# Kernel tuning notes

Measured on AMD Instinct MI355X. Metric: run time of the kernel, lower is better.

The kernel has to match this reference:

```python
import jax, jax.numpy as jnp
import numpy as np

B, T = 1, 1024
V, E, H, HKV, DH = 32000, 1024, 16, 4, 64
L, R = 2, 2            # n_layer, n_recurrent
ROPE = 32              # head_dim * rotary_pct (0.5)
EPS = 1e-5


def _layer_norm(x, g, b):
    mu = jnp.mean(x, axis=-1, keepdims=True)
    var = jnp.mean((x - mu) ** 2, axis=-1, keepdims=True)
    return (x - mu) * jax.lax.rsqrt(var + EPS) * g + b


def _rotate_half(x):
    x1, x2 = jnp.split(x, 2, axis=-1)
    return jnp.concatenate([-x2, x1], axis=-1)


def _rope_cache(t):
    theta = 1.0 / (10000.0 ** (jnp.arange(0, ROPE, 2, dtype=jnp.float32) / ROPE))
    freqs = jnp.arange(t, dtype=jnp.float32)[:, None] * theta[None, :]  # [t, ROPE/2]
    cos = jnp.concatenate([jnp.cos(freqs), jnp.cos(freqs)], axis=-1)    # [t, ROPE]
    sin = jnp.concatenate([jnp.sin(freqs), jnp.sin(freqs)], axis=-1)
    return cos, sin


def _attn(x, Wq, Wk, Wv, Wo, gate, cos, sin):
    b, t, c = x.shape
    q = (x @ Wq).reshape(b, t, H, DH).transpose(0, 2, 1, 3)     # [b,H,t,D]
    k = (x @ Wk).reshape(b, t, HKV, DH).transpose(0, 2, 1, 3)   # [b,Hkv,t,D]
    v = (x @ Wv).reshape(b, t, HKV, DH).transpose(0, 2, 1, 3)
    c4, s4 = cos[None, None, :t, :], sin[None, None, :t, :]
    q_r, q_p = q[..., :ROPE], q[..., ROPE:]
    k_r, k_p = k[..., :ROPE], k[..., ROPE:]
    q = jnp.concatenate([q_r * c4 + _rotate_half(q_r) * s4, q_p], axis=-1)
    k = jnp.concatenate([k_r * c4 + _rotate_half(k_r) * s4, k_p], axis=-1)
    # GQA: repeat kv heads
    k = jnp.repeat(k, H // HKV, axis=1)
    v = jnp.repeat(v, H // HKV, axis=1)
    att = jnp.einsum('bhtd,bhsd->bhts', q, k) * (DH ** -0.5)
    causal = jnp.tril(jnp.ones((t, t), dtype=bool))
    att = jnp.where(causal[None, None], att, -jnp.inf)
    att = jax.nn.softmax(att, axis=-1)
    # learned per-head sigmoid-threshold sparsifying gate
    thr = jax.nn.sigmoid(gate)[None, :, None, None]
    att = att * (att >= thr).astype(att.dtype)
    y = jnp.einsum('bhts,bhsd->bhtd', att, v).transpose(0, 2, 1, 3).reshape(b, t, c)
    return y @ Wo


def reference(embed, ln1_g, ln1_b, Wq, Wk, Wv, Wo, gate, ln2_g, ln2_b, W1, W2, lnf_g, lnf_b, idx, targets):
    x = embed[idx]                      # [B,T,E]
    cos, sin = _rope_cache(T)
    for _ in range(R):
        for l in range(L):
            x = x + _attn(_layer_norm(x, ln1_g[l], ln1_b[l]), Wq[l], Wk[l], Wv[l], Wo[l], gate[l], cos, sin)
            h = _layer_norm(x, ln2_g[l], ln2_b[l])
            x = x + jax.nn.gelu(h @ W1[l], approximate=False) @ W2[l]
    x = _layer_norm(x, lnf_g, lnf_b)
    logits = x @ embed.T                # tied lm_head
    logp = jax.nn.log_softmax(logits, axis=-1)
    loss = -jnp.mean(jnp.take_along_axis(logp, targets[..., None], axis=-1))
    return logits, loss


def setup_inputs():
    key = jax.random.key(0)
    ks = jax.random.split(key, 9)
    s = 0.02
    return {
        'embed': jax.random.normal(ks[0], (V, E), jnp.float32) * s,
        'ln1_g': jnp.ones((L, E), jnp.float32), 'ln1_b': jnp.zeros((L, E), jnp.float32),
        'Wq': jax.random.normal(ks[1], (L, E, E), jnp.float32) * s,
        'Wk': jax.random.normal(ks[2], (L, E, HKV * DH), jnp.float32) * s,
        'Wv': jax.random.normal(ks[3], (L, E, HKV * DH), jnp.float32) * s,
        'Wo': jax.random.normal(ks[4], (L, E, E), jnp.float32) * s,
        'gate': jnp.zeros((L, H), jnp.float32),
        'ln2_g': jnp.ones((L, E), jnp.float32), 'ln2_b': jnp.zeros((L, E), jnp.float32),
        'W1': jax.random.normal(ks[5], (L, E, 4 * E), jnp.float32) * s,
        'W2': jax.random.normal(ks[6], (L, 4 * E, E), jnp.float32) * s,
        'lnf_g': jnp.ones((E,), jnp.float32), 'lnf_b': jnp.zeros((E,), jnp.float32),
        'idx': jax.random.randint(ks[7], (B, T), 0, V, dtype=jnp.int32),
        'targets': jax.random.randint(ks[8], (B, T), 0, V, dtype=jnp.int32),
    }
```

## Files before the change

kernel.cpp:

```cpp
#include <hip/hip_runtime.h>
#include <math.h>

#define TT 1024
#define VV 32000
#define EE 1024
#define NH 16
#define NKVH 4
#define DHEAD 64
#define QKVN 1536
#define FF 4096
#define LEPS 1e-5f

typedef __attribute__((ext_vector_type(8))) short short8;
typedef __attribute__((ext_vector_type(4))) float floatx4;

__device__ __forceinline__ ushort f2bf(float f) {
    unsigned x = __float_as_uint(f);
    unsigned r = (x + 0x7fffu + ((x >> 16) & 1u)) >> 16;
    return (ushort)r;
}
__device__ __forceinline__ float bf2f(ushort u) {
    return __uint_as_float(((unsigned)u) << 16);
}

__device__ __forceinline__ float block_reduce_sum(float v, float* red) {
    int tid = threadIdx.x;
    red[tid] = v; __syncthreads();
    for (int off = 128; off > 0; off >>= 1) {
        if (tid < off) red[tid] += red[tid + off];
        __syncthreads();
    }
    float r = red[0];
    __syncthreads();
    return r;
}
__device__ __forceinline__ float block_reduce_max(float v, float* red) {
    int tid = threadIdx.x;
    red[tid] = v; __syncthreads();
    for (int off = 128; off > 0; off >>= 1) {
        if (tid < off) red[tid] = fmaxf(red[tid], red[tid + off]);
        __syncthreads();
    }
    float r = red[0];
    __syncthreads();
    return r;
}

__global__ __launch_bounds__(256) void convert_bf16_kernel(const float* __restrict__ src,
                                                           ushort* __restrict__ dst, long n4) {
    long i = (long)blockIdx.x * 256 + threadIdx.x;
    if (i >= n4) return;
    float4 f = ((const float4*)src)[i];
    ushort u[4] = { f2bf(f.x), f2bf(f.y), f2bf(f.z), f2bf(f.w) };
    ((uint2*)dst)[i] = *(uint2*)u;
}

__global__ __launch_bounds__(256) void transpose_bf16_kernel(const float* __restrict__ W,
                                                             ushort* __restrict__ dst,
                                                             int N, int K) {
    __shared__ float tile[32][33];
    int n0 = blockIdx.x * 32, k0 = blockIdx.y * 32;
    int tx = threadIdx.x & 31, ty = threadIdx.x >> 5;
    for (int i = ty; i < 32; i += 8) tile[i][tx] = W[(long)(k0 + i) * N + n0 + tx];
    __syncthreads();
    for (int i = ty; i < 32; i += 8)
        dst[(long)(n0 + i) * K + k0 + tx] = f2bf(tile[tx][i]);
}

__global__ __launch_bounds__(256) void gather_kernel(const float* __restrict__ embed,
                                                     const int* __restrict__ idx,
                                                     float* __restrict__ x) {
    int t = blockIdx.x;
    long r = idx[t];
    const float4* src = (const float4*)(embed + r * EE);
    float4* dst = (float4*)(x + (long)t * EE);
    for (int i = threadIdx.x; i < EE / 4; i += 256) dst[i] = src[i];
}

__global__ __launch_bounds__(256) void ln_kernel(const float* __restrict__ x,
                                                 const float* __restrict__ g,
                                                 const float* __restrict__ b,
                                                 ushort* __restrict__ out) {
    __shared__ float red[256];
    int t = blockIdx.x;
    const float* xr = x + (long)t * EE;
    float s = 0.f;
    for (int i = threadIdx.x; i < EE; i += 256) s += xr[i];
    float mu = block_reduce_sum(s, red) * (1.f / EE);
    float vs = 0.f;
    for (int i = threadIdx.x; i < EE; i += 256) { float d = xr[i] - mu; vs += d * d; }
    float var = block_reduce_sum(vs, red) * (1.f / EE);
    float rstd = rsqrtf(var + LEPS);
    ushort* orow = out + (long)t * EE;
    for (int i = threadIdx.x; i < EE; i += 256)
        orow[i] = f2bf((xr[i] - mu) * rstd * g[i] + b[i]);
}

__global__ __launch_bounds__(256) void rope_kernel(ushort* __restrict__ q, int nheads, int rowstride) {
    int idx = blockIdx.x * 256 + threadIdx.x;
    int total = TT * nheads * 16;
    if (idx >= total) return;
    int i = idx & 15;
    int h = (idx >> 4) % nheads;
    int t = idx / (16 * nheads);
    float theta = expf(-(float)i * (9.210340371976184f / 16.f));
    float ang = (float)t * theta;
    float c = cosf(ang), s = sinf(ang);
    ushort* p = q + (long)t * rowstride + h * DHEAD;
    float a = bf2f(p[i]), bb = bf2f(p[i + 16]);
    p[i]      = f2bf(a * c - bb * s);
    p[i + 16] = f2bf(bb * c + a * s);
}

template<bool GELU_ACT, bool ADD, bool OUTBF>
__global__ __launch_bounds__(256) void gemm_bf16(const ushort* __restrict__ A,
                                                 const ushort* __restrict__ B,
                                                 void* __restrict__ Cv,
                                                 int M, int N, int K) {
    __shared__ char lds[16384];
    const int tid = threadIdx.x;
    const int lane = tid & 63;
    const int w = tid >> 6;

    const int nwg = gridDim.x;
    const int lin = blockIdx.x;
    const int q8 = nwg >> 3, r8 = nwg & 7;
    const int xcd = lin & 7, loc = lin >> 3;
    const int wg = (xcd < r8 ? xcd * (q8 + 1) : r8 * (q8 + 1) + (xcd - r8) * q8) + loc;
    const int MB = M >> 7;
    const int row0 = (wg % MB) * 128;
    const int col0 = (wg / MB) * 128;

    const int nsl = gridDim.y;
    const int kslice = K / nsl;
    const long koff = (long)blockIdx.y * kslice;

    const char* ga[2]; const char* gb[2];
    char* la[2]; char* lb[2];
    #pragma unroll
    for (int r = 0; r < 2; ++r) {
        int c = r * 256 + tid;
        ga[r] = (const char*)A + ((long)(row0 + (c >> 2)) * K + koff) * 2 + (c & 3) * 16;
        gb[r] = (const char*)B + ((long)(col0 + (c >> 2)) * K + koff) * 2 + (c & 3) * 16;
        int wc = r * 256 + w * 64;
        la[r] = lds + wc * 16;
        lb[r] = lds + 8192 + wc * 16;
    }

    floatx4 acc[4][4];
    #pragma unroll
    for (int i = 0; i < 4; ++i)
        #pragma unroll
        for (int j = 0; j < 4; ++j) acc[i][j] = {0.f, 0.f, 0.f, 0.f};

    const int mbase = (w >> 1) * 64;
    const int nbase = (w & 1) * 64;
    const int lr = lane & 15;
    const int ko = (lane >> 4) * 16;

    for (int k0 = 0; k0 < kslice; k0 += 32) {
        #pragma unroll
        for (int r = 0; r < 2; ++r) {
            __builtin_amdgcn_global_load_lds(
                (const __attribute__((address_space(1))) void*)ga[r],
                (__attribute__((address_space(3))) void*)la[r], 16, 0, 0);
            __builtin_amdgcn_global_load_lds(
                (const __attribute__((address_space(1))) void*)gb[r],
                (__attribute__((address_space(3))) void*)lb[r], 16, 0, 0);
            ga[r] += 64; gb[r] += 64;
        }
        __syncthreads();
        short8 af[4], bfr[4];
        #pragma unroll
        for (int i = 0; i < 4; ++i)
            af[i] = *(const short8*)(lds + (mbase + i * 16 + lr) * 64 + ko);
        #pragma unroll
        for (int j = 0; j < 4; ++j)
            bfr[j] = *(const short8*)(lds + 8192 + (nbase + j * 16 + lr) * 64 + ko);
        #pragma unroll
        for (int i = 0; i < 4; ++i)
            #pragma unroll
            for (int j = 0; j < 4; ++j)
                acc[i][j] = __builtin_amdgcn_mfma_f32_16x16x32_bf16(af[i], bfr[j], acc[i][j], 0, 0, 0);
        __syncthreads();
    }

    const int orow = (lane >> 4) * 4;
    const int ocol = lane & 15;
    #pragma unroll
    for (int i = 0; i < 4; ++i) {
        #pragma unroll
        for (int j = 0; j < 4; ++j) {
            #pragma unroll
            for (int r = 0; r < 4; ++r) {
                long off = (long)(row0 + mbase + i * 16 + orow + r) * N
                         + (col0 + nbase + j * 16 + ocol);
                float v = acc[i][j][r];
                if (GELU_ACT) v = 0.5f * v * (1.f + erff(v * 0.70710678118654752f));
                if (OUTBF) {
                    ((ushort*)Cv)[off] = f2bf(v);
                } else {
                    float* C = (float*)Cv + (long)blockIdx.y * (long)M * N;
                    if (ADD) C[off] += v; else C[off] = v;
                }
            }
        }
    }
}

__global__ __launch_bounds__(256) void reduce_add_kernel(const float* __restrict__ part,
                                                         float* __restrict__ x,
                                                         long n4, int SK) {
    long i = (long)blockIdx.x * 256 + threadIdx.x;
    if (i >= n4) return;
    float4 s = ((const float4*)part)[i];
    for (int k = 1; k < SK; ++k) {
        float4 t = ((const float4*)part)[i + (long)k * n4];
        s.x += t.x; s.y += t.y; s.z += t.z; s.w += t.w;
    }
    float4 d = ((float4*)x)[i];
    d.x += s.x; d.y += s.y; d.z += s.z; d.w += s.w;
    ((float4*)x)[i] = d;
}

__global__ __launch_bounds__(256) void scores_gemm(const ushort* __restrict__ qkv,
                                                   float* __restrict__ scores) {
    __shared__ char lds[16384];
    const int tid = threadIdx.x;
    const int lane = tid & 63;
    const int w = tid >> 6;
    const int col0 = blockIdx.x * 128, row0 = blockIdx.y * 128, h = blockIdx.z;
    if (col0 > row0) return;

    const ushort* A = qkv + h * DHEAD;
    const ushort* B = qkv + EE + (h >> 2) * DHEAD;

    const char* ga[2]; const char* gb[2];
    char* la[2]; char* lb[2];
    #pragma unroll
    for (int r = 0; r < 2; ++r) {
        int c = r * 256 + tid;
        ga[r] = (const char*)A + (long)(row0 + (c >> 2)) * QKVN * 2 + (c & 3) * 16;
        gb[r] = (const char*)B + (long)(col0 + (c >> 2)) * QKVN * 2 + (c & 3) * 16;
        int wc = r * 256 + w * 64;
        la[r] = lds + wc * 16;
        lb[r] = lds + 8192 + wc * 16;
    }

    floatx4 acc[4][4];
    #pragma unroll
    for (int i = 0; i < 4; ++i)
        #pragma unroll
        for (int j = 0; j < 4; ++j) acc[i][j] = {0.f, 0.f, 0.f, 0.f};

    const int mbase = (w >> 1) * 64;
    const int nbase = (w & 1) * 64;
    const int lr = lane & 15;
    const int ko = (lane >> 4) * 16;

    for (int k0 = 0; k0 < DHEAD; k0 += 32) {
        #pragma unroll
        for (int r = 0; r < 2; ++r) {
            __builtin_amdgcn_global_load_lds(
                (const __attribute__((address_space(1))) void*)ga[r],
                (__attribute__((address_space(3))) void*)la[r], 16, 0, 0);
            __builtin_amdgcn_global_load_lds(
                (const __attribute__((address_space(1))) void*)gb[r],
                (__attribute__((address_space(3))) void*)lb[r], 16, 0, 0);
            ga[r] += 64; gb[r] += 64;
        }
        __syncthreads();
        short8 af[4], bfr[4];
        #pragma unroll
        for (int i = 0; i < 4; ++i)
            af[i] = *(const short8*)(lds + (mbase + i * 16 + lr) * 64 + ko);
        #pragma unroll
        for (int j = 0; j < 4; ++j)
            bfr[j] = *(const short8*)(lds + 8192 + (nbase + j * 16 + lr) * 64 + ko);
        #pragma unroll
        for (int i = 0; i < 4; ++i)
            #pragma unroll
            for (int j = 0; j < 4; ++j)
                acc[i][j] = __builtin_amdgcn_mfma_f32_16x16x32_bf16(af[i], bfr[j], acc[i][j], 0, 0, 0);
        __syncthreads();
    }

    float* C = scores + (long)h * TT * TT;
    const int orow = (lane >> 4) * 4;
    const int ocol = lane & 15;
    #pragma unroll
    for (int i = 0; i < 4; ++i)
        #pragma unroll
        for (int j = 0; j < 4; ++j)
            #pragma unroll
            for (int r = 0; r < 4; ++r)
                C[(long)(row0 + mbase + i * 16 + orow + r) * TT
                  + (col0 + nbase + j * 16 + ocol)] = acc[i][j][r];
}

__global__ __launch_bounds__(256) void softmax_gate_kernel(float* __restrict__ scores,
                                                           const float* __restrict__ gate) {
    __shared__ float sc[TT];
    __shared__ float red[256];
    int h = blockIdx.x;
    int t = blockIdx.y;
    int tid = threadIdx.x;
    float* row = scores + (long)h * TT * TT + (long)t * TT;

    float lmax = -INFINITY;
    for (int s = tid; s <= t; s += 256) {
        float v = row[s] * 0.125f;
        sc[s] = v;
        lmax = fmaxf(lmax, v);
    }
    float mx = block_reduce_max(lmax, red);
    float lsum = 0.f;
    for (int s = tid; s <= t; s += 256) {
        float e = expf(sc[s] - mx);
        sc[s] = e;
        lsum += e;
    }
    float sum = block_reduce_sum(lsum, red);
    float inv = 1.f / sum;
    float thr = 1.f / (1.f + expf(-gate[h]));

    ushort* prow = (ushort*)row;
    for (int s = tid; s < TT; s += 256) {
        float p = (s <= t) ? sc[s] * inv : 0.f;
        p = (p >= thr) ? p : 0.f;
        prow[s] = f2bf(p);
    }
}

__global__ __launch_bounds__(256) void vtrans_kernel(const ushort* __restrict__ qkv,
                                                     ushort* __restrict__ VT) {
    __shared__ ushort tile[32][33];
    int s0 = blockIdx.x * 32, d0 = blockIdx.y * 32;
    int tx = threadIdx.x & 31, ty = threadIdx.x >> 5;
    for (int i = ty; i < 32; i += 8)
        tile[i][tx] = qkv[(long)(s0 + i) * QKVN + (EE + NKVH * DHEAD) + d0 + tx];
    __syncthreads();
    for (int i = ty; i < 32; i += 8)
        VT[(long)(d0 + i) * TT + s0 + tx] = tile[tx][i];
}

__global__ __launch_bounds__(256) void pv_gemm(const float* __restrict__ scores,
                                               const ushort* __restrict__ VT,
                                               ushort* __restrict__ y) {
    __shared__ char lds[12288];
    const int tid = threadIdx.x;
    const int lane = tid & 63;
    const int w = tid >> 6;
    const int row0 = blockIdx.x * 128, h = blockIdx.y;

    const char* Pb = (const char*)(scores + (long)h * TT * TT);
    const char* Bv = (const char*)(VT + (long)(h >> 2) * DHEAD * TT);

    const char* ga[2]; char* la[2];
    #pragma unroll
    for (int r = 0; r < 2; ++r) {
        int c = r * 256 + tid;
        ga[r] = Pb + (long)(row0 + (c >> 2)) * 4096 + (c & 3) * 16;
        la[r] = lds + (r * 256 + w * 64) * 16;
    }
    const char* gb = Bv + (long)(tid >> 2) * 2048 + (tid & 3) * 16;
    char* lb = lds + 8192 + (w * 64) * 16;

    floatx4 acc[2][4];
    #pragma unroll
    for (int i = 0; i < 2; ++i)
        #pragma unroll
        for (int j = 0; j < 4; ++j) acc[i][j] = {0.f, 0.f, 0.f, 0.f};

    const int mbase = w * 32;
    const int lr = lane & 15;
    const int ko = (lane >> 4) * 16;

    for (int k0 = 0; k0 < TT; k0 += 32) {
        #pragma unroll
        for (int r = 0; r < 2; ++r) {
            __builtin_amdgcn_global_load_lds(
                (const __attribute__((address_space(1))) void*)ga[r],
                (__attribute__((address_space(3))) void*)la[r], 16, 0, 0);
            ga[r] += 64;
        }
        __builtin_amdgcn_global_load_lds(
            (const __attribute__((address_space(1))) void*)gb,
            (__attribute__((address_space(3))) void*)lb, 16, 0, 0);
        gb += 64;
        __syncthreads();
        short8 af[2], bfr[4];
        #pragma unroll
        for (int i = 0; i < 2; ++i)
            af[i] = *(const short8*)(lds + (mbase + i * 16 + lr) * 64 + ko);
        #pragma unroll
        for (int j = 0; j < 4; ++j)
            bfr[j] = *(const short8*)(lds + 8192 + (j * 16 + lr) * 64 + ko);
        #pragma unroll
        for (int i = 0; i < 2; ++i)
            #pragma unroll
            for (int j = 0; j < 4; ++j)
                acc[i][j] = __builtin_amdgcn_mfma_f32_16x16x32_bf16(af[i], bfr[j], acc[i][j], 0, 0, 0);
        __syncthreads();
    }

    const int orow = (lane >> 4) * 4;
    const int ocol = lane & 15;
    #pragma unroll
    for (int i = 0; i < 2; ++i)
        #pragma unroll
        for (int j = 0; j < 4; ++j)
            #pragma unroll
            for (int r = 0; r < 4; ++r)
                y[(long)(row0 + mbase + i * 16 + orow + r) * EE
                  + h * DHEAD + j * 16 + ocol] = f2bf(acc[i][j][r]);
}

__global__ __launch_bounds__(256) void row_loss_kernel(const float* __restrict__ logits,
                                                       const int* __restrict__ targets,
                                                       float* __restrict__ row_loss) {
    __shared__ float red[256];
    int t = blockIdx.x;
    const float* lr = logits + (long)t * VV;
    float lmax = -INFINITY;
    for (int i = threadIdx.x; i < VV; i += 256) lmax = fmaxf(lmax, lr[i]);
    float mx = block_reduce_max(lmax, red);
    float ls = 0.f;
    for (int i = threadIdx.x; i < VV; i += 256) ls += expf(lr[i] - mx);
    float sum = block_reduce_sum(ls, red);
    if (threadIdx.x == 0)
        row_loss[t] = logf(sum) + mx - lr[targets[t]];
}

__global__ __launch_bounds__(256) void final_loss_kernel(const float* __restrict__ row_loss,
                                                         float* __restrict__ out) {
    __shared__ float red[256];
    float s = 0.f;
    for (int i = threadIdx.x; i < TT; i += 256) s += row_loss[i];
    float tot = block_reduce_sum(s, red);
    if (threadIdx.x == 0) out[0] = tot * (1.f / TT);
}

extern "C" void kernel_launch(void* const* d_in, const int* in_sizes, int n_in,
                              void* d_out, int out_size, void* d_ws, size_t ws_size,
                              hipStream_t stream) {
    const float* embed = (const float*)d_in[0];
    const float* ln1_g = (const float*)d_in[1];
    const float* ln1_b = (const float*)d_in[2];
    const float* Wq    = (const float*)d_in[3];
    const float* Wk    = (const float*)d_in[4];
    const float* Wv    = (const float*)d_in[5];
    const float* Wo    = (const float*)d_in[6];
    const float* gate  = (const float*)d_in[7];
    const float* ln2_g = (const float*)d_in[8];
    const float* ln2_b = (const float*)d_in[9];
    const float* W1    = (const float*)d_in[10];
    const float* W2    = (const float*)d_in[11];
    const float* lnf_g = (const float*)d_in[12];
    const float* lnf_b = (const float*)d_in[13];
    const int*   idx   = (const int*)d_in[14];
    const int*   tgt   = (const int*)d_in[15];
    float* out = (float*)d_out;

    char* p = (char*)d_ws;
    float*  x      = (float*)p;  p += (long)TT * EE * 4;
    ushort* xn     = (ushort*)p; p += (long)TT * EE * 2;
    ushort* qkvb   = (ushort*)p; p += (long)TT * QKVN * 2;
    ushort* y      = (ushort*)p; p += (long)TT * EE * 2;
    ushort* h1     = (ushort*)p; p += (long)TT * FF * 2;
    float*  rls    = (float*)p;  p += (long)TT * 4;
    ushort* VT     = (ushort*)p; p += (long)NKVH * DHEAD * TT * 2;
    float*  scores = (float*)p;  p += (long)NH * TT * TT * 4;
    ushort* wqkvT  = (ushort*)p; p += (long)2 * QKVN * EE * 2;
    ushort* woT    = (ushort*)p; p += (long)2 * EE * EE * 2;
    ushort* w1T    = (ushort*)p; p += (long)2 * FF * EE * 2;
    ushort* w2T    = (ushort*)p; p += (long)2 * EE * FF * 2;
    ushort* embB   = (ushort*)p; p += (long)VV * EE * 2;

    float* gpart = scores;

    convert_bf16_kernel<<<((long)VV * EE / 4 + 255) / 256, 256, 0, stream>>>(embed, embB, (long)VV * EE / 4);
    for (int l = 0; l < 2; ++l) {
        transpose_bf16_kernel<<<dim3(EE / 32, EE / 32), 256, 0, stream>>>(
            Wq + (long)l * EE * EE, wqkvT + (long)l * QKVN * EE, EE, EE);
        transpose_bf16_kernel<<<dim3(NKVH * DHEAD / 32, EE / 32), 256, 0, stream>>>(
            Wk + (long)l * EE * NKVH * DHEAD, wqkvT + (long)l * QKVN * EE + (long)EE * EE, NKVH * DHEAD, EE);
        transpose_bf16_kernel<<<dim3(NKVH * DHEAD / 32, EE / 32), 256, 0, stream>>>(
            Wv + (long)l * EE * NKVH * DHEAD, wqkvT + (long)l * QKVN * EE + (long)(EE + NKVH * DHEAD) * EE, NKVH * DHEAD, EE);
        transpose_bf16_kernel<<<dim3(EE / 32, EE / 32), 256, 0, stream>>>(
            Wo + (long)l * EE * EE, woT + (long)l * EE * EE, EE, EE);
        transpose_bf16_kernel<<<dim3(FF / 32, EE / 32), 256, 0, stream>>>(
            W1 + (long)l * EE * FF, w1T + (long)l * FF * EE, FF, EE);
        transpose_bf16_kernel<<<dim3(EE / 32, FF / 32), 256, 0, stream>>>(
            W2 + (long)l * FF * EE, w2T + (long)l * EE * FF, EE, FF);
    }

    gather_kernel<<<TT, 256, 0, stream>>>(embed, idx, x);

    for (int r = 0; r < 2; ++r) {
        for (int l = 0; l < 2; ++l) {
            ln_kernel<<<TT, 256, 0, stream>>>(x, ln1_g + l * EE, ln1_b + l * EE, xn);
            gemm_bf16<false, false, true><<<dim3((TT / 128) * (QKVN / 128)), 256, 0, stream>>>(
                xn, wqkvT + (long)l * QKVN * EE, qkvb, TT, QKVN, EE);
            rope_kernel<<<(TT * NH * 16 + 255) / 256, 256, 0, stream>>>(qkvb, NH, QKVN);
            rope_kernel<<<(TT * NKVH * 16 + 255) / 256, 256, 0, stream>>>(qkvb + EE, NKVH, QKVN);
            vtrans_kernel<<<dim3(TT / 32, NKVH * DHEAD / 32), 256, 0, stream>>>(qkvb, VT);
            scores_gemm<<<dim3(TT / 128, TT / 128, NH), 256, 0, stream>>>(qkvb, scores);
            softmax_gate_kernel<<<dim3(NH, TT), 256, 0, stream>>>(scores, gate + l * NH);
            pv_gemm<<<dim3(TT / 128, NH), 256, 0, stream>>>(scores, VT, y);

            gemm_bf16<false, false, false><<<dim3((TT / 128) * (EE / 128), 2), 256, 0, stream>>>(
                y, woT + (long)l * EE * EE, gpart, TT, EE, EE);
            reduce_add_kernel<<<(TT * EE / 4 + 255) / 256, 256, 0, stream>>>(
                gpart, x, (long)TT * EE / 4, 2);

            ln_kernel<<<TT, 256, 0, stream>>>(x, ln2_g + l * EE, ln2_b + l * EE, xn);
            gemm_bf16<true, false, true><<<dim3((TT / 128) * (FF / 128)), 256, 0, stream>>>(
                xn, w1T + (long)l * FF * EE, h1, TT, FF, EE);

            gemm_bf16<false, false, false><<<dim3((TT / 128) * (EE / 128), 4), 256, 0, stream>>>(
                h1, w2T + (long)l * EE * FF, gpart, TT, EE, FF);
            reduce_add_kernel<<<(TT * EE / 4 + 255) / 256, 256, 0, stream>>>(
                gpart, x, (long)TT * EE / 4, 4);
        }
    }

    ln_kernel<<<TT, 256, 0, stream>>>(x, lnf_g, lnf_b, xn);
    gemm_bf16<false, false, false><<<dim3((TT / 128) * (VV / 128)), 256, 0, stream>>>(
        xn, embB, out, TT, VV, EE);

    row_loss_kernel<<<TT, 256, 0, stream>>>(out, tgt, rls);
    final_loss_kernel<<<1, 256, 0, stream>>>(rls, out + (long)TT * VV);
}
```

Measured before the change: 1.298 ms.

## Fuse RoPE, residual+LayerNorm, and LM-head softmax stats into neighbouring kernels

Applies RoPE in the QKV GEMM epilogue, removing the separate rope kernels. Merges the split-K residual reduction with the following LayerNorm. Computes per-tile max/sum-exp statistics in the LM-head GEMM epilogue, so the loss kernel no longer rereads the full logits. It also rewrites softmax to one wavefront per row with shuffle reductions and truncates the PV GEMM loop at the causal boundary. Together these cut launches and full-tensor memory passes, at the cost of heavier GEMM epilogues and more complex code.

Result: faster. 1.186 ms (-8.6%).

```diff
diff --git a/kernel.cpp b/kernel.cpp
--- a/kernel.cpp
+++ b/kernel.cpp
@@ -96,26 +96,46 @@
         orow[i] = f2bf((xr[i] - mu) * rstd * g[i] + b[i]);
 }
 
-__global__ __launch_bounds__(256) void rope_kernel(ushort* __restrict__ q, int nheads, int rowstride) {
-    int idx = blockIdx.x * 256 + threadIdx.x;
-    int total = TT * nheads * 16;
-    if (idx >= total) return;
-    int i = idx & 15;
-    int h = (idx >> 4) % nheads;
-    int t = idx / (16 * nheads);
-    float theta = expf(-(float)i * (9.210340371976184f / 16.f));
-    float ang = (float)t * theta;
-    float c = cosf(ang), s = sinf(ang);
-    ushort* p = q + (long)t * rowstride + h * DHEAD;
-    float a = bf2f(p[i]), bb = bf2f(p[i + 16]);
-    p[i]      = f2bf(a * c - bb * s);
-    p[i + 16] = f2bf(bb * c + a * s);
-}
-
-template<bool GELU_ACT, bool ADD, bool OUTBF>
+__global__ __launch_bounds__(256) void reduce_ln_kernel(const float* __restrict__ part,
+                                                        float* __restrict__ x,
+                                                        const float* __restrict__ g,
+                                                        const float* __restrict__ b,
+                                                        ushort* __restrict__ out, int SK) {
+    __shared__ float red[256];
+    int t = blockIdx.x;
+    int tid = threadIdx.x;
+    float4 v = ((const float4*)(x + (long)t * EE))[tid];
+    for (int k = 0; k < SK; ++k) {
+        float4 pp = ((const float4*)(part + (long)k * TT * EE + (long)t * EE))[tid];
+        v.x += pp.x; v.y += pp.y; v.z += pp.z; v.w += pp.w;
+    }
+    ((float4*)(x + (long)t * EE))[tid] = v;
+    float s = v.x + v.y + v.z + v.w;
+    float mu = block_reduce_sum(s, red) * (1.f / EE);
+    float d0 = v.x - mu, d1 = v.y - mu, d2 = v.z - mu, d3 = v.w - mu;
+    float vs = d0 * d0 + d1 * d1 + d2 * d2 + d3 * d3;
+    float var = block_reduce_sum(vs, red) * (1.f / EE);
+    float rstd = rsqrtf(var + LEPS);
+    float4 gg = ((const float4*)g)[tid];
+    float4 bb = ((const float4*)b)[tid];
+    ushort4 o;
+    o.x = f2bf(d0 * rstd * gg.x + bb.x);
+    o.y = f2bf(d1 * rstd * gg.y + bb.y);
+    o.z = f2bf(d2 * rstd * gg.z + bb.z);
+    o.w = f2bf(d3 * rstd * gg.w + bb.w);
+    ((ushort4*)(out + (long)t * EE))[tid] = o;
+}
+
+#define M_QKV    0
+#define M_FF1    1
+#define M_PART   2
+#define M_LMHEAD 3
+
+template<int MODE>
 __global__ __launch_bounds__(256) void gemm_bf16(const ushort* __restrict__ A,
                                                  const ushort* __restrict__ B,
                                                  void* __restrict__ Cv,
+                                                 float* __restrict__ lstats,
                                                  int M, int N, int K) {
     __shared__ char lds[16384];
     const int tid = threadIdx.x;
@@ -187,6 +207,21 @@
 
     const int orow = (lane >> 4) * 4;
     const int ocol = lane & 15;
+
+    if (MODE == M_QKV && (col0 + nbase) < (EE + NKVH * DHEAD)) {
+        float th = expf(-(float)ocol * 0.5756462732485114f);
+        #pragma unroll
+        for (int i = 0; i < 4; ++i)
+            #pragma unroll
+            for (int r = 0; r < 4; ++r) {
+                float ang = (float)(row0 + mbase + i * 16 + orow + r) * th;
+                float c = cosf(ang), s = sinf(ang);
+                float a = acc[i][0][r], bb = acc[i][1][r];
+                acc[i][0][r] = a * c - bb * s;
+                acc[i][1][r] = bb * c + a * s;
+            }
+    }
+
     #pragma unroll
     for (int i = 0; i < 4; ++i) {
         #pragma unroll
@@ -196,31 +231,55 @@
                 long off = (long)(row0 + mbase + i * 16 + orow + r) * N
                          + (col0 + nbase + j * 16 + ocol);
                 float v = acc[i][j][r];
-                if (GELU_ACT) v = 0.5f * v * (1.f + erff(v * 0.70710678118654752f));
-                if (OUTBF) {
+                if (MODE == M_FF1) v = 0.5f * v * (1.f + erff(v * 0.70710678118654752f));
+                if (MODE == M_QKV || MODE == M_FF1) {
                     ((ushort*)Cv)[off] = f2bf(v);
                 } else {
-                    float* C = (float*)Cv + (long)blockIdx.y * (long)M * N;
-                    if (ADD) C[off] += v; else C[off] = v;
+                    ((float*)Cv + (long)blockIdx.y * (long)M * N)[off] = v;
                 }
             }
         }
     }
-}
-
-__global__ __launch_bounds__(256) void reduce_add_kernel(const float* __restrict__ part,
-                                                         float* __restrict__ x,
-                                                         long n4, int SK) {
-    long i = (long)blockIdx.x * 256 + threadIdx.x;
-    if (i >= n4) return;
-    float4 s = ((const float4*)part)[i];
-    for (int k = 1; k < SK; ++k) {
-        float4 t = ((const float4*)part)[i + (long)k * n4];
-        s.x += t.x; s.y += t.y; s.z += t.z; s.w += t.w;
-    }
-    float4 d = ((float4*)x)[i];
-    d.x += s.x; d.y += s.y; d.z += s.z; d.w += s.w;
-    ((float4*)x)[i] = d;
+
+    if (MODE == M_LMHEAD) {
+        float rm[4][4], rs[4][4];
+        #pragma unroll
+        for (int i = 0; i < 4; ++i)
+            #pragma unroll
+            for (int r = 0; r < 4; ++r) {
+                float m0 = fmaxf(fmaxf(acc[i][0][r], acc[i][1][r]),
+                                 fmaxf(acc[i][2][r], acc[i][3][r]));
+                float s0 = expf(acc[i][0][r] - m0) + expf(acc[i][1][r] - m0)
+                         + expf(acc[i][2][r] - m0) + expf(acc[i][3][r] - m0);
+                #pragma unroll
+                for (int off = 1; off < 16; off <<= 1) {
+                    float om = __shfl_xor(m0, off);
+                    float os = __shfl_xor(s0, off);
+                    float nm = fmaxf(m0, om);
+                    s0 = s0 * expf(m0 - nm) + os * expf(om - nm);
+                    m0 = nm;
+                }
+                rm[i][r] = m0; rs[i][r] = s0;
+            }
+        float2* msb = (float2*)lds;
+        if (ocol == 0) {
+            #pragma unroll
+            for (int i = 0; i < 4; ++i)
+                #pragma unroll
+                for (int r = 0; r < 4; ++r)
+                    msb[w * 64 + i * 16 + orow + r] = make_float2(rm[i][r], rs[i][r]);
+        }
+        __syncthreads();
+        if (tid < 128) {
+            int half = tid >> 6, rloc = tid & 63;
+            float2 a = msb[(half * 2) * 64 + rloc];
+            float2 bq = msb[(half * 2 + 1) * 64 + rloc];
+            float nm = fmaxf(a.x, bq.x);
+            float ns = a.y * expf(a.x - nm) + bq.y * expf(bq.x - nm);
+            ((float2*)lstats)[(long)(row0 + half * 64 + rloc) * (N >> 7) + (col0 >> 7)]
+                = make_float2(nm, ns);
+        }
+    }
 }
 
 __global__ __launch_bounds__(256) void scores_gemm(const ushort* __restrict__ qkv,
@@ -300,35 +359,54 @@
 
 __global__ __launch_bounds__(256) void softmax_gate_kernel(float* __restrict__ scores,
                                                            const float* __restrict__ gate) {
-    __shared__ float sc[TT];
-    __shared__ float red[256];
     int h = blockIdx.x;
-    int t = blockIdx.y;
-    int tid = threadIdx.x;
+    int t = blockIdx.y * 4 + (threadIdx.x >> 6);
+    int lane = threadIdx.x & 63;
     float* row = scores + (long)h * TT * TT + (long)t * TT;
 
+    float4 v[4];
     float lmax = -INFINITY;
-    for (int s = tid; s <= t; s += 256) {
-        float v = row[s] * 0.125f;
-        sc[s] = v;
-        lmax = fmaxf(lmax, v);
-    }
-    float mx = block_reduce_max(lmax, red);
+    #pragma unroll
+    for (int q = 0; q < 4; ++q) {
+        int u = lane + q * 64;
+        v[q] = ((const float4*)row)[u];
+        int s0 = u * 4;
+        v[q].x = (s0 + 0 <= t) ? v[q].x * 0.125f : -INFINITY;
+        v[q].y = (s0 + 1 <= t) ? v[q].y * 0.125f : -INFINITY;
+        v[q].z = (s0 + 2 <= t) ? v[q].z * 0.125f : -INFINITY;
+        v[q].w = (s0 + 3 <= t) ? v[q].w * 0.125f : -INFINITY;
+        lmax = fmaxf(lmax, fmaxf(fmaxf(v[q].x, v[q].y), fmaxf(v[q].z, v[q].w)));
+    }
+    #pragma unroll
+    for (int off = 1; off < 64; off <<= 1)
+        lmax = fmaxf(lmax, __shfl_xor(lmax, off));
+
+    float e[16];
     float lsum = 0.f;
-    for (int s = tid; s <= t; s += 256) {
-        float e = expf(sc[s] - mx);
-        sc[s] = e;
-        lsum += e;
-    }
-    float sum = block_reduce_sum(lsum, red);
-    float inv = 1.f / sum;
+    #pragma unroll
+    for (int q = 0; q < 4; ++q) {
+        e[q * 4 + 0] = expf(v[q].x - lmax);
+        e[q * 4 + 1] = expf(v[q].y - lmax);
+        e[q * 4 + 2] = expf(v[q].z - lmax);
+        e[q * 4 + 3] = expf(v[q].w - lmax);
+        lsum += e[q * 4 + 0] + e[q * 4 + 1] + e[q * 4 + 2] + e[q * 4 + 3];
+    }
+    #pragma unroll
+    for (int off = 1; off < 64; off <<= 1)
+        lsum += __shfl_xor(lsum, off);
+
+    float inv = 1.f / lsum;
     float thr = 1.f / (1.f + expf(-gate[h]));
-
     ushort* prow = (ushort*)row;
-    for (int s = tid; s < TT; s += 256) {
-        float p = (s <= t) ? sc[s] * inv : 0.f;
-        p = (p >= thr) ? p : 0.f;
-        prow[s] = f2bf(p);
+    #pragma unroll
+    for (int q = 0; q < 4; ++q) {
+        ushort4 o;
+        float p;
+        p = e[q * 4 + 0] * inv; o.x = f2bf(p >= thr ? p : 0.f);
+        p = e[q * 4 + 1] * inv; o.y = f2bf(p >= thr ? p : 0.f);
+        p = e[q * 4 + 2] * inv; o.z = f2bf(p >= thr ? p : 0.f);
+        p = e[q * 4 + 3] * inv; o.w = f2bf(p >= thr ? p : 0.f);
+        ((ushort4*)prow)[lane + q * 64] = o;
     }
 }
 
@@ -376,7 +454,8 @@
     const int lr = lane & 15;
     const int ko = (lane >> 4) * 16;
 
-    for (int k0 = 0; k0 < TT; k0 += 32) {
+    const int kmax = row0 + 128;
+    for (int k0 = 0; k0 < kmax; k0 += 32) {
         #pragma unroll
         for (int r = 0; r < 2; ++r) {
             __builtin_amdgcn_global_load_lds(
@@ -416,20 +495,30 @@
                   + h * DHEAD + j * 16 + ocol] = f2bf(acc[i][j][r]);
 }
 
-__global__ __launch_bounds__(256) void row_loss_kernel(const float* __restrict__ logits,
-                                                       const int* __restrict__ targets,
-                                                       float* __restrict__ row_loss) {
-    __shared__ float red[256];
+__global__ __launch_bounds__(64) void row_loss_kernel(const float* __restrict__ logits,
+                                                      const float* __restrict__ lstats,
+                                                      const int* __restrict__ targets,
+                                                      float* __restrict__ row_loss) {
     int t = blockIdx.x;
-    const float* lr = logits + (long)t * VV;
-    float lmax = -INFINITY;
-    for (int i = threadIdx.x; i < VV; i += 256) lmax = fmaxf(lmax, lr[i]);
-    float mx = block_reduce_max(lmax, red);
-    float ls = 0.f;
-    for (int i = threadIdx.x; i < VV; i += 256) ls += expf(lr[i] - mx);
-    float sum = block_reduce_sum(ls, red);
-    if (threadIdx.x == 0)
-        row_loss[t] = logf(sum) + mx - lr[targets[t]];
+    int lane = threadIdx.x;
+    const float2* st = (const float2*)lstats + (long)t * (VV / 128);
+    float m = -INFINITY, s = 0.f;
+    for (int i = lane; i < VV / 128; i += 64) {
+        float2 v = st[i];
+        float nm = fmaxf(m, v.x);
+        s = s * expf(m - nm) + v.y * expf(v.x - nm);
+        m = nm;
+    }
+    #pragma unroll
+    for (int off = 1; off < 64; off <<= 1) {
+        float om = __shfl_xor(m, off);
+        float os = __shfl_xor(s, off);
+        float nm = fmaxf(m, om);
+        s = s * expf(m - nm) + os * expf(om - nm);
+        m = nm;
+    }
+    if (lane == 0)
+        row_loss[t] = logf(s) + m - logits[(long)t * VV + targets[t]];
 }
 
 __global__ __launch_bounds__(256) void final_loss_kernel(const float* __restrict__ row_loss,
@@ -496,39 +585,37 @@
     }
 
     gather_kernel<<<TT, 256, 0, stream>>>(embed, idx, x);
+    ln_kernel<<<TT, 256, 0, stream>>>(x, ln1_g, ln1_b, xn);
 
     for (int r = 0; r < 2; ++r) {
         for (int l = 0; l < 2; ++l) {
-            ln_kernel<<<TT, 256, 0, stream>>>(x, ln1_g + l * EE, ln1_b + l * EE, xn);
-            gemm_bf16<false, false, true><<<dim3((TT / 128) * (QKVN / 128)), 256, 0, stream>>>(
-                xn, wqkvT + (long)l * QKVN * EE, qkvb, TT, QKVN, EE);
-            rope_kernel<<<(TT * NH * 16 + 255) / 256, 256, 0, stream>>>(qkvb, NH, QKVN);
-            rope_kernel<<<(TT * NKVH * 16 + 255) / 256, 256, 0, stream>>>(qkvb + EE, NKVH, QKVN);
+            gemm_bf16<M_QKV><<<dim3((TT / 128) * (QKVN / 128)), 256, 0, stream>>>(
+                xn, wqkvT + (long)l * QKVN * EE, qkvb, nullptr, TT, QKVN, EE);
             vtrans_kernel<<<dim3(TT / 32, NKVH * DHEAD / 32), 256, 0, stream>>>(qkvb, VT);
             scores_gemm<<<dim3(TT / 128, TT / 128, NH), 256, 0, stream>>>(qkvb, scores);
-            softmax_gate_kernel<<<dim3(NH, TT), 256, 0, stream>>>(scores, gate + l * NH);
+            softmax_gate_kernel<<<dim3(NH, TT / 4), 256, 0, stream>>>(scores, gate + l * NH);
             pv_gemm<<<dim3(TT / 128, NH), 256, 0, stream>>>(scores, VT, y);
 
-            gemm_bf16<false, false, false><<<dim3((TT / 128) * (EE / 128), 2), 256, 0, stream>>>(
-                y, woT + (long)l * EE * EE, gpart, TT, EE, EE);
-            reduce_add_kernel<<<(TT * EE / 4 + 255) / 256, 256, 0, stream>>>(
-                gpart, x, (long)TT * EE / 4, 2);
-
-            ln_kernel<<<TT, 256, 0, stream>>>(x, ln2_g + l * EE, ln2_b + l * EE, xn);
-            gemm_bf16<true, false, true><<<dim3((TT / 128) * (FF / 128)), 256, 0, stream>>>(
-                xn, w1T + (long)l * FF * EE, h1, TT, FF, EE);
-
-            gemm_bf16<false, false, false><<<dim3((TT / 128) * (EE / 128), 4), 256, 0, stream>>>(
-                h1, w2T + (long)l * EE * FF, gpart, TT, EE, FF);
-            reduce_add_kernel<<<(TT * EE / 4 + 255) / 256, 256, 0, stream>>>(
-                gpart, x, (long)TT * EE / 4, 4);
+            gemm_bf16<M_PART><<<dim3((TT / 128) * (EE / 128), 2), 256, 0, stream>>>(
+                y, woT + (long)l * EE * EE, gpart, nullptr, TT, EE, EE);
+            reduce_ln_kernel<<<TT, 256, 0, stream>>>(
+                gpart, x, ln2_g + l * EE, ln2_b + l * EE, xn, 2);
+
+            gemm_bf16<M_FF1><<<dim3((TT / 128) * (FF / 128)), 256, 0, stream>>>(
+                xn, w1T + (long)l * FF * EE, h1, nullptr, TT, FF, EE);
+
+            gemm_bf16<M_PART><<<dim3((TT / 128) * (EE / 128), 4), 256, 0, stream>>>(
+                h1, w2T + (long)l * EE * FF, gpart, nullptr, TT, EE, FF);
+            const float* gn; const float* bn;
+            if (r == 1 && l == 1) { gn = lnf_g; bn = lnf_b; }
+            else { int lnx = (l == 0) ? 1 : 0; gn = ln1_g + lnx * EE; bn = ln1_b + lnx * EE; }
+            reduce_ln_kernel<<<TT, 256, 0, stream>>>(gpart, x, gn, bn, xn, 4);
         }
     }
 
-    ln_kernel<<<TT, 256, 0, stream>>>(x, lnf_g, lnf_b, xn);
-    gemm_bf16<false, false, false><<<dim3((TT / 128) * (VV / 128)), 256, 0, stream>>>(
-        xn, embB, out, TT, VV, EE);
-
-    row_loss_kernel<<<TT, 256, 0, stream>>>(out, tgt, rls);
+    gemm_bf16<M_LMHEAD><<<dim3((TT / 128) * (VV / 128)), 256, 0, stream>>>(
+        xn, embB, out, gpart, TT, VV, EE);
+
+    row_loss_kernel<<<TT, 64, 0, stream>>>(out, gpart, tgt, rls);
     final_loss_kernel<<<1, 256, 0, stream>>>(rls, out + (long)TT * VV);
 }
```
